# Kernel tuning notes

Hardware: AMD Instinct MI355X
Metric: run time of the kernel (lower is better)

The kernel has to match this reference:

```python
import jax, jax.numpy as jnp
import numpy as np

N = 4096
IN_SIZE = 512
MLP_W = 16
HID = 512
MID = 64  # hardcoded tgc2 output size in the torch module
OUT = 128
BN_EPS = 1e-5


def setup_inputs() -> dict:
    key = jax.random.key(0)
    ks = jax.random.split(key, 24)
    adj = (jax.random.uniform(ks[0], (N, N)) < 0.05).astype(jnp.float32)
    xdeg = jax.random.uniform(ks[1], (N, N), dtype=jnp.float32)
    ydeg = jax.random.uniform(ks[2], (N, N), dtype=jnp.float32)
    u = lambda k, sh, fan: jax.random.uniform(k, sh, jnp.float32, -1.0, 1.0) / np.sqrt(fan)
    return {
        "adj": adj, "xdeg": xdeg, "ydeg": ydeg,
        # edge MLP: 3 -> MLP_W -> 2
        "mlp_w1": u(ks[3], (3, MLP_W), 3), "mlp_b1": jnp.zeros((MLP_W,), jnp.float32),
        "mlp_w2": u(ks[4], (MLP_W, 2), MLP_W), "mlp_b2": jnp.zeros((2,), jnp.float32),
        # positional linear: Linear(N, in_size) applied to eye(N) -> pe = W^T + b
        "pe_w": u(ks[5], (N, IN_SIZE), N), "pe_b": jnp.zeros((IN_SIZE,), jnp.float32),
        # GCN weights
        "gc1_w": u(ks[6], (IN_SIZE, HID), HID),
        "lin2_w": u(ks[7], (HID, MID), HID), "lin2_b": jnp.zeros((MID,), jnp.float32),
        "gc3_w": u(ks[8], (MID, OUT), OUT),
        # BatchNorm (eval mode: running stats)
        "bn1_g": jnp.ones((HID,), jnp.float32), "bn1_b": jnp.zeros((HID,), jnp.float32),
        "bn1_m": jnp.zeros((HID,), jnp.float32), "bn1_v": jnp.ones((HID,), jnp.float32),
        "bn2_g": jnp.ones((OUT,), jnp.float32), "bn2_b": jnp.zeros((OUT,), jnp.float32),
        "bn2_m": jnp.zeros((OUT,), jnp.float32), "bn2_v": jnp.ones((OUT,), jnp.float32),
    }


def reference(adj, xdeg, ydeg, mlp_w1, mlp_b1, mlp_w2, mlp_b2, pe_w, pe_b,
              gc1_w, lin2_w, lin2_b, gc3_w,
              bn1_g, bn1_b, bn1_m, bn1_v, bn2_g, bn2_b, bn2_m, bn2_v):
    # Edge MLP + softmax over [adj, xdeg, ydeg] features; torch only computes it
    # at nonzero adj entries then scatters into a dense mask. Since the mask is
    # multiplied by adj, computing densely and multiplying is exactly equivalent.
    feats = jnp.stack([adj, xdeg, ydeg], axis=-1)          # [N, N, 3]
    h = jax.nn.relu(jnp.einsum('nmf,fw->nmw', feats, mlp_w1) + mlp_b1)
    logits = jnp.einsum('nmw,wc->nmc', h, mlp_w2) + mlp_b2  # [N, N, 2]
    mask = jax.nn.softmax(logits, axis=-1)[..., 1]          # [N, N]
    a = adj * mask + jnp.eye(adj.shape[0], dtype=adj.dtype)

    # Degree normalization: A' = D_row^{-1/2} A D_col^{-1/2} (broadcast, no diag matmuls)
    rowsum = jnp.sum(a, axis=1)
    colsum = jnp.sum(a, axis=0)
    d_row = jnp.where(rowsum > 0, rowsum ** -0.5, 0.0)
    d_col = jnp.where(colsum > 0, colsum ** -0.5, 0.0)
    a = d_row[:, None] * a * d_col[None, :]

    # pe = Linear(eye(N)) = W^T + b (eval mode, dropout off)
    pe = pe_w + pe_b[None, :]                               # [N, IN_SIZE]

    h = a @ (pe @ gc1_w)                                    # GCN layer 1
    h = (h - bn1_m) * (bn1_g / jnp.sqrt(bn1_v + BN_EPS)) + bn1_b
    h = h @ lin2_w + lin2_b                                 # tgc2
    mid = h
    h = jax.nn.relu(h)
    h = a @ (h @ gc3_w)                                     # GCN layer 3
    out = (h - bn2_m) * (bn2_g / jnp.sqrt(bn2_v + BN_EPS)) + bn2_b
    return out, mid
```

## Files before the change

### kernel.cpp

```cpp
#include <hip/hip_runtime.h>
#include <hip/hip_bf16.h>

#define NN 4096
#define INS 512
#define HIDW 512
#define MIDW 64
#define OUTW 128
#define CAP 384
#define SEG 96
#define BN_EPS 1e-5f
#define CS_BLOCKS 256
#define CS_ROWS (NN / CS_BLOCKS)
#define NSTRIP 8

__global__ __launch_bounds__(256) void k_count(
    const float* __restrict__ adj,
    unsigned long long* __restrict__ msk, int* __restrict__ cnt,
    int* __restrict__ dflag)
{
    const int t = threadIdx.x;
    const int wave = t >> 6, lane = t & 63;
    const int gw = blockIdx.x * 4 + wave;
    const int i = gw >> 3, s = gw & 7;
    const int colbase = s * 512;
    const float* __restrict__ base = adj + (size_t)i * NN + colbase + 4 * lane;
    float4 a4a = *reinterpret_cast<const float4*>(base);
    float4 a4b = *reinterpret_cast<const float4*>(base + 256);
    const float av[8] = {a4a.x, a4a.y, a4a.z, a4a.w,
                         a4b.x, a4b.y, a4b.z, a4b.w};
    unsigned long long m[8];
    int total = 0;
    #pragma unroll
    for (int c = 0; c < 8; ++c) {
        int col = colbase + ((c < 4) ? (4 * lane + c) : (256 + 4 * lane + c - 4));
        bool diag = (col == i);
        bool act = (av[c] != 0.f) || diag;
        if (diag) dflag[i] = (av[c] != 0.f) ? 1 : 0;
        m[c] = __ballot(act);
        total += __popcll(m[c]);
    }
    if (lane == 0) {
        unsigned long long* mp = msk + (size_t)gw * 8;
        #pragma unroll
        for (int c = 0; c < 8; ++c) mp[c] = m[c];
        cnt[gw] = total;
    }
}

__global__ __launch_bounds__(256) void k_fill(
    const float* __restrict__ xdeg, const float* __restrict__ ydeg,
    const unsigned long long* __restrict__ msk, const int* __restrict__ cnt,
    const int* __restrict__ dflag,
    const float* __restrict__ w1, const float* __restrict__ b1,
    const float* __restrict__ w2, const float* __restrict__ b2,
    float* __restrict__ a_vals, int* __restrict__ a_cols,
    float* __restrict__ rs_part)
{
    __shared__ float shb[16], sw1x[16], sw1y[16], sw2[32], sb2[2];
    __shared__ int   scol[4][SEG];
    __shared__ float sx[4][SEG];
    __shared__ float sy[4][SEG];
    const int t = threadIdx.x;
    const int wave = t >> 6, lane = t & 63;
    if (t < 16) {
        shb[t]  = b1[t] + w1[t];
        sw1x[t] = w1[16 + t];
        sw1y[t] = w1[32 + t];
    }
    if (t < 32) sw2[t] = w2[t];
    if (t < 2)  sb2[t] = b2[t];
    __syncthreads();

    const int gw = __builtin_amdgcn_readfirstlane(blockIdx.x * 4 + wave);
    const int i = gw >> 3, s = gw & 7;
    const int colbase = s * 512;
    const size_t rbase = (size_t)i * NN + colbase + 4 * lane;
    float4 x4a = *reinterpret_cast<const float4*>(xdeg + rbase);
    float4 x4b = *reinterpret_cast<const float4*>(xdeg + rbase + 256);
    float4 y4a = *reinterpret_cast<const float4*>(ydeg + rbase);
    float4 y4b = *reinterpret_cast<const float4*>(ydeg + rbase + 256);
    const unsigned long long* __restrict__ mp = msk + (size_t)gw * 8;
    unsigned long long mm[8];
    #pragma unroll
    for (int c = 0; c < 8; ++c) mm[c] = mp[c];
    const int* __restrict__ cb = cnt + i * NSTRIP;
    int wb = 0;
    #pragma unroll
    for (int ss = 0; ss < NSTRIP; ++ss) if (ss < s) wb += cb[ss];
    const int hasde = dflag[i];

    int bases[8];
    bases[0] = 0;
    #pragma unroll
    for (int c = 1; c < 8; ++c) bases[c] = bases[c - 1] + __popcll(mm[c - 1]);
    const int cnt_ = bases[7] + __popcll(mm[7]);
    const int n = (cnt_ < SEG) ? cnt_ : SEG;
    const unsigned long long lt = (1ULL << lane) - 1ULL;

    const float xv[8] = {x4a.x, x4a.y, x4a.z, x4a.w,
                         x4b.x, x4b.y, x4b.z, x4b.w};
    const float yv[8] = {y4a.x, y4a.y, y4a.z, y4a.w,
                         y4b.x, y4b.y, y4b.z, y4b.w};
    #pragma unroll
    for (int c = 0; c < 8; ++c) {
        if ((mm[c] >> lane) & 1ULL) {
            int pos = bases[c] + __popcll(mm[c] & lt);
            if (pos < SEG) {
                scol[wave][pos] = colbase + ((c < 4) ? (4 * lane + c)
                                                     : (256 + 4 * lane + c - 4));
                sx[wave][pos] = xv[c];
                sy[wave][pos] = yv[c];
            }
        }
    }

    float* __restrict__ gv = a_vals + (size_t)i * CAP;
    int*   __restrict__ gc = a_cols + (size_t)i * CAP;
    float local = 0.f;
    for (int p = lane; p < n; p += 64) {
        int col = scol[wave][p];
        float x = sx[wave][p], y = sy[wave][p];
        float l0 = sb2[0], l1 = sb2[1];
        #pragma unroll
        for (int w = 0; w < 16; ++w) {
            float hw = fmaf(x, sw1x[w], shb[w]);
            hw = fmaf(y, sw1y[w], hw);
            hw = fmaxf(hw, 0.f);
            l0 = fmaf(hw, sw2[2 * w],     l0);
            l1 = fmaf(hw, sw2[2 * w + 1], l1);
        }
        float v = 1.f / (1.f + __expf(l0 - l1));
        if (col == i) v = hasde ? (v + 1.f) : 1.f;
        int gp = wb + p;
        if (gp < CAP) { gc[gp] = col; gv[gp] = v; }
        local += v;
    }
    #pragma unroll
    for (int o = 32; o >= 1; o >>= 1)
        local += __shfl_down(local, o, 64);
    if (lane == 0) rs_part[gw] = local;
}

__global__ __launch_bounds__(256) void k_colsum(
    const float* __restrict__ a_vals, const int* __restrict__ a_cols,
    const int* __restrict__ cnt, float* __restrict__ P)
{
    __shared__ float ls[NN];
    const int t = threadIdx.x;
    const int b = blockIdx.x;
    for (int j = t; j < NN; j += 256) ls[j] = 0.f;
    __syncthreads();
    const int r0 = b * CS_ROWS;
    for (int r = r0; r < r0 + CS_ROWS; ++r) {
        int n = 0;
        #pragma unroll
        for (int ss = 0; ss < NSTRIP; ++ss) n += cnt[r * NSTRIP + ss];
        n = (n < CAP) ? n : CAP;
        const float* __restrict__ vr = a_vals + (size_t)r * CAP;
        const int*   __restrict__ cr = a_cols + (size_t)r * CAP;
        for (int p = t; p < n; p += 256)
            atomicAdd(&ls[cr[p]], vr[p]);
    }
    __syncthreads();
    for (int j = t; j < NN; j += 256)
        P[(size_t)b * NN + j] = ls[j];
}

__global__ __launch_bounds__(512) void k_misc(
    const float* __restrict__ lin2_w, const float* __restrict__ lin2_b,
    const float* __restrict__ bn1_g, const float* __restrict__ bn1_b,
    const float* __restrict__ bn1_m, const float* __restrict__ bn1_v,
    const float* __restrict__ bn2_g, const float* __restrict__ bn2_b,
    const float* __restrict__ bn2_m, const float* __restrict__ bn2_v,
    const float* __restrict__ rs_part, const float* __restrict__ P,
    float* __restrict__ Wp, float* __restrict__ c1,
    float* __restrict__ s2g, float* __restrict__ t2g,
    float* __restrict__ d_row, float* __restrict__ d_col)
{
    const int t = threadIdx.x;
    if (blockIdx.x == 0) {
        __shared__ float t1s[HIDW];
        {
            int h = t;
            float s1 = bn1_g[h] * rsqrtf(bn1_v[h] + BN_EPS);
            t1s[h] = bn1_b[h] - bn1_m[h] * s1;
            for (int m = 0; m < MIDW; ++m)
                Wp[(size_t)h * MIDW + m] = s1 * lin2_w[(size_t)h * MIDW + m];
        }
        __syncthreads();
        if (t < MIDW) {
            float acc = lin2_b[t];
            for (int h = 0; h < HIDW; ++h)
                acc = fmaf(t1s[h], lin2_w[(size_t)h * MIDW + t], acc);
            c1[t] = acc;
        } else if (t >= 64 && t < 64 + OUTW) {
            int j = t - 64;
            float s2 = bn2_g[j] * rsqrtf(bn2_v[j] + BN_EPS);
            s2g[j] = s2;
            t2g[j] = bn2_b[j] - bn2_m[j] * s2;
        }
    } else {
        int j = (blockIdx.x - 1) * 512 + t;
        float r = 0.f;
        #pragma unroll
        for (int s = 0; s < NSTRIP; ++s) r += rs_part[j * NSTRIP + s];
        d_row[j] = (r > 0.f) ? 1.f / sqrtf(r) : 0.f;
        float c = 0.f;
        for (int b = 0; b < CS_BLOCKS; ++b)
            c += P[(size_t)b * NN + j];
        d_col[j] = (c > 0.f) ? 1.f / sqrtf(c) : 0.f;
    }
}

template <bool ABIAS, bool ROWSCALE>
__global__ __launch_bounds__(256) void k_thin(
    const float* __restrict__ A, const float* __restrict__ B,
    const float* __restrict__ abias, const float* __restrict__ rscale,
    float* __restrict__ C, int M, int K)
{
    __shared__ float As[64][36];
    __shared__ float Bs[64][64];
    const int t = threadIdx.x;
    const int bm = blockIdx.x * 32;
    const int c2 = t & 31, rg = t >> 5;

    float acc[4][2] = {};

    for (int k0 = 0; k0 < K; k0 += 64) {
        #pragma unroll
        for (int l = 0; l < 8; ++l) {
            int e = t + l * 256;
            int r = e >> 6, k = e & 63;
            float v = A[(size_t)(bm + r) * K + k0 + k];
            if (ABIAS) v += abias[k0 + k];
            As[k][r] = v;
        }
        #pragma unroll
        for (int l = 0; l < 16; ++l) {
            int e = t + l * 256;
            int k = e >> 6, n = e & 63;
            Bs[k][n] = B[(size_t)(k0 + k) * 64 + n];
        }
        __syncthreads();
        #pragma unroll
        for (int k = 0; k < 64; ++k) {
            float4 a4 = *reinterpret_cast<const float4*>(&As[k][rg * 4]);
            float2 b2 = *reinterpret_cast<const float2*>(&Bs[k][2 * c2]);
            acc[0][0] = fmaf(a4.x, b2.x, acc[0][0]);
            acc[0][1] = fmaf(a4.x, b2.y, acc[0][1]);
            acc[1][0] = fmaf(a4.y, b2.x, acc[1][0]);
            acc[1][1] = fmaf(a4.y, b2.y, acc[1][1]);
            acc[2][0] = fmaf(a4.z, b2.x, acc[2][0]);
            acc[2][1] = fmaf(a4.z, b2.y, acc[2][1]);
            acc[3][0] = fmaf(a4.w, b2.x, acc[3][0]);
            acc[3][1] = fmaf(a4.w, b2.y, acc[3][1]);
        }
        __syncthreads();
    }

    #pragma unroll
    for (int u = 0; u < 4; ++u) {
        int r = bm + rg * 4 + u;
        float sc = ROWSCALE ? rscale[r] : 1.f;
        float2 o = make_float2(acc[u][0] * sc, acc[u][1] * sc);
        *reinterpret_cast<float2*>(&C[(size_t)r * 64 + 2 * c2]) = o;
    }
}

template <bool WITH_MID>
__global__ __launch_bounds__(256) void k_spmm(
    const float* __restrict__ a_vals, const int* __restrict__ a_cols,
    const int* __restrict__ cnt, const float* __restrict__ X,
    const float* __restrict__ d_row, const float* __restrict__ d_col,
    const float* __restrict__ c1,
    const float* __restrict__ gc3, const float* __restrict__ s2g,
    const float* __restrict__ t2g,
    float* __restrict__ O1, float* __restrict__ O2)
{
    __shared__ float sv[2][CAP];
    __shared__ int   scl[2][CAP];
    __shared__ float sacc[4][64];
    const int t = threadIdx.x;
    const int wave = t >> 6, lane = t & 63;
    const int rb = wave >> 1, h = wave & 1;
    const int i = blockIdx.x * 2 + rb;
    int n = 0;
    #pragma unroll
    for (int ss = 0; ss < NSTRIP; ++ss) n += cnt[i * NSTRIP + ss];
    n = (n < CAP) ? n : CAP;
    const int n16 = (n + 15) & ~15;
    const float* __restrict__ vrow = a_vals + (size_t)i * CAP;
    const int*   __restrict__ crow = a_cols + (size_t)i * CAP;

    for (int p = h * 64 + lane; p < n16; p += 128) {
        bool ok = p < n;
        sv[rb][p]  = ok ? vrow[p] : 0.f;
        scl[rb][p] = ok ? crow[p] : 0;
    }
    __syncthreads();

    const int eh = lane >> 5;
    const int lc = lane & 31;
    const int Q  = n16 >> 1;
    const int Qh = Q >> 1;

    float a0 = 0.f, a1 = 0.f;
    for (int q = h * Qh; q < (h + 1) * Qh; q += 4) {
        #pragma unroll
        for (int j = 0; j < 4; ++j) {
            int p = 2 * (q + j) + eh;
            float v = sv[rb][p];
            int c = scl[rb][p];
            float2 x = *reinterpret_cast<const float2*>(X + (size_t)c * 64 + 2 * lc);
            a0 = fmaf(v, x.x, a0);
            a1 = fmaf(v, x.y, a1);
        }
    }
    a0 += __shfl_xor(a0, 32);
    a1 += __shfl_xor(a1, 32);
    if (lane < 32) { sacc[wave][2 * lc] = a0; sacc[wave][2 * lc + 1] = a1; }
    __syncthreads();

    if (WITH_MID) {
        if (h == 0 && lane < 32) {
            float s0 = sacc[wave][2 * lc]     + sacc[wave + 1][2 * lc];
            float s1 = sacc[wave][2 * lc + 1] + sacc[wave + 1][2 * lc + 1];
            float dr = d_row[i];
            float dc = d_col[i];
            float m0 = fmaf(s0, dr, c1[2 * lc]);
            float m1 = fmaf(s1, dr, c1[2 * lc + 1]);
            *reinterpret_cast<float2*>(O1 + (size_t)i * 64 + 2 * lc) =
                make_float2(m0, m1);
            *reinterpret_cast<float2*>(O2 + (size_t)i * 64 + 2 * lc) =
                make_float2(dc * fmaxf(m0, 0.f), dc * fmaxf(m1, 0.f));
        }
    } else {
        if (h == 0 && lane < 32) {
            float dr = d_row[i];
            float s0 = (sacc[wave][2 * lc]     + sacc[wave + 1][2 * lc])     * dr;
            float s1 = (sacc[wave][2 * lc + 1] + sacc[wave + 1][2 * lc + 1]) * dr;
            sacc[wave][2 * lc]     = s0;
            sacc[wave][2 * lc + 1] = s1;
        }
        __syncthreads();
        const int rb2 = t >> 7;
        const int j = t & 127;
        const float* __restrict__ srow = sacc[2 * rb2];
        float acc = 0.f;
        #pragma unroll 8
        for (int k = 0; k < 64; ++k)
            acc = fmaf(srow[k], gc3[k * 128 + j], acc);
        int orow = blockIdx.x * 2 + rb2;
        O1[(size_t)orow * 128 + j] = fmaf(acc, s2g[j], t2g[j]);
    }
}

extern "C" void kernel_launch(void* const* d_in, const int* in_sizes, int n_in,
                              void* d_out, int out_size, void* d_ws, size_t ws_size,
                              hipStream_t stream) {
    const float* adj    = (const float*)d_in[0];
    const float* xdeg   = (const float*)d_in[1];
    const float* ydeg   = (const float*)d_in[2];
    const float* mlp_w1 = (const float*)d_in[3];
    const float* mlp_b1 = (const float*)d_in[4];
    const float* mlp_w2 = (const float*)d_in[5];
    const float* mlp_b2 = (const float*)d_in[6];
    const float* pe_w   = (const float*)d_in[7];
    const float* pe_b   = (const float*)d_in[8];
    const float* gc1_w  = (const float*)d_in[9];
    const float* lin2_w = (const float*)d_in[10];
    const float* lin2_b = (const float*)d_in[11];
    const float* gc3_w  = (const float*)d_in[12];
    const float* bn1_g  = (const float*)d_in[13];
    const float* bn1_b  = (const float*)d_in[14];
    const float* bn1_m  = (const float*)d_in[15];
    const float* bn1_v  = (const float*)d_in[16];
    const float* bn2_g  = (const float*)d_in[17];
    const float* bn2_b  = (const float*)d_in[18];
    const float* bn2_m  = (const float*)d_in[19];
    const float* bn2_v  = (const float*)d_in[20];

    float* out = (float*)d_out;
    float* mid = out + (size_t)NN * OUTW;

    char* w = (char*)d_ws;
    float* a_vals = (float*)w;  w += (size_t)NN * CAP * 4;
    int*   a_cols = (int*)w;    w += (size_t)NN * CAP * 4;
    unsigned long long* msk = (unsigned long long*)w; w += (size_t)NN * NSTRIP * 8 * 8;
    int*   cnt    = (int*)w;    w += (size_t)NN * NSTRIP * 4;
    int*   dflag  = (int*)w;    w += (size_t)NN * 4;
    float* rs_part= (float*)w;  w += (size_t)NN * NSTRIP * 4;
    float* d_row  = (float*)w;  w += (size_t)NN * 4;
    float* d_col  = (float*)w;  w += (size_t)NN * 4;
    float* P      = (float*)w;  w += (size_t)CS_BLOCKS * NN * 4;
    float* Wp     = (float*)w;  w += (size_t)HIDW * MIDW * 4;
    float* W2     = (float*)w;  w += (size_t)INS * MIDW * 4;
    float* c1     = (float*)w;  w += 256;
    float* s2g    = (float*)w;  w += 512;
    float* t2g    = (float*)w;  w += 512;
    float* G      = (float*)w;  w += (size_t)NN * MIDW * 4;
    float* R      = (float*)w;  w += (size_t)NN * MIDW * 4;

    k_count<<<NN * NSTRIP / 4, 256, 0, stream>>>(adj, msk, cnt, dflag);
    k_fill<<<NN * NSTRIP / 4, 256, 0, stream>>>(
        xdeg, ydeg, msk, cnt, dflag, mlp_w1, mlp_b1, mlp_w2, mlp_b2,
        a_vals, a_cols, rs_part);
    k_colsum<<<CS_BLOCKS, 256, 0, stream>>>(a_vals, a_cols, cnt, P);
    k_misc<<<9, 512, 0, stream>>>(lin2_w, lin2_b, bn1_g, bn1_b, bn1_m, bn1_v,
                                  bn2_g, bn2_b, bn2_m, bn2_v, rs_part, P,
                                  Wp, c1, s2g, t2g, d_row, d_col);
    k_thin<false, false><<<INS / 32, 256, 0, stream>>>(
        gc1_w, Wp, nullptr, nullptr, W2, INS, HIDW);
    k_thin<true, true><<<NN / 32, 256, 0, stream>>>(
        pe_w, W2, pe_b, d_col, G, NN, INS);
    k_spmm<true><<<NN / 2, 256, 0, stream>>>(
        a_vals, a_cols, cnt, G, d_row, d_col, c1,
        nullptr, nullptr, nullptr, mid, R);
    k_spmm<false><<<NN / 2, 256, 0, stream>>>(
        a_vals, a_cols, cnt, R, d_row, d_col, nullptr,
        gc3_w, s2g, t2g, out, nullptr);
}
```

Before: 135.9 us.

## Compact nonzero column indices in count pass and gather xdeg/ydeg sparsely

The count kernel now writes compacted per-strip column indices directly into a slot buffer instead of ballot bitmasks. The fill kernel uses those indices to gather xdeg and ydeg values only at active columns, rather than streaming full dense rows and compacting them through shared memory. The aim is to cut dense read traffic on the two large feature matrices. In exchange, the reads become scattered and uncoalesced, and at about 5% density most cache lines may still be touched. Strip counts are now stored capped at SEG, which changes the row write offsets slightly.

```diff
diff --git a/kernel.cpp b/kernel.cpp
--- a/kernel.cpp
+++ b/kernel.cpp
@@ -12,11 +12,11 @@
 #define CS_BLOCKS 256
 #define CS_ROWS (NN / CS_BLOCKS)
 #define NSTRIP 8
+#define SLOTCAP (NSTRIP * SEG)
 
 __global__ __launch_bounds__(256) void k_count(
     const float* __restrict__ adj,
-    unsigned long long* __restrict__ msk, int* __restrict__ cnt,
-    int* __restrict__ dflag)
+    int* __restrict__ cslot, int* __restrict__ cnt, int* __restrict__ dflag)
 {
     const int t = threadIdx.x;
     const int wave = t >> 6, lane = t & 63;
@@ -28,28 +28,28 @@
     float4 a4b = *reinterpret_cast<const float4*>(base + 256);
     const float av[8] = {a4a.x, a4a.y, a4a.z, a4a.w,
                          a4b.x, a4b.y, a4b.z, a4b.w};
-    unsigned long long m[8];
-    int total = 0;
+    int* __restrict__ slot = cslot + (size_t)i * SLOTCAP + s * SEG;
+    const unsigned long long lt = (1ULL << lane) - 1ULL;
+    int run = 0;
     #pragma unroll
     for (int c = 0; c < 8; ++c) {
         int col = colbase + ((c < 4) ? (4 * lane + c) : (256 + 4 * lane + c - 4));
         bool diag = (col == i);
         bool act = (av[c] != 0.f) || diag;
         if (diag) dflag[i] = (av[c] != 0.f) ? 1 : 0;
-        m[c] = __ballot(act);
-        total += __popcll(m[c]);
-    }
-    if (lane == 0) {
-        unsigned long long* mp = msk + (size_t)gw * 8;
-        #pragma unroll
-        for (int c = 0; c < 8; ++c) mp[c] = m[c];
-        cnt[gw] = total;
-    }
+        unsigned long long m = __ballot(act);
+        if (act) {
+            int pos = run + __popcll(m & lt);
+            if (pos < SEG) slot[pos] = col;
+        }
+        run += __popcll(m);
+    }
+    if (lane == 0) cnt[gw] = (run < SEG) ? run : SEG;
 }
 
 __global__ __launch_bounds__(256) void k_fill(
     const float* __restrict__ xdeg, const float* __restrict__ ydeg,
-    const unsigned long long* __restrict__ msk, const int* __restrict__ cnt,
+    const int* __restrict__ cslot, const int* __restrict__ cnt,
     const int* __restrict__ dflag,
     const float* __restrict__ w1, const float* __restrict__ b1,
     const float* __restrict__ w2, const float* __restrict__ b2,
@@ -57,9 +57,6 @@
     float* __restrict__ rs_part)
 {
     __shared__ float shb[16], sw1x[16], sw1y[16], sw2[32], sb2[2];
-    __shared__ int   scol[4][SEG];
-    __shared__ float sx[4][SEG];
-    __shared__ float sy[4][SEG];
     const int t = threadIdx.x;
     const int wave = t >> 6, lane = t & 63;
     if (t < 16) {
@@ -73,53 +70,23 @@
 
     const int gw = __builtin_amdgcn_readfirstlane(blockIdx.x * 4 + wave);
     const int i = gw >> 3, s = gw & 7;
-    const int colbase = s * 512;
-    const size_t rbase = (size_t)i * NN + colbase + 4 * lane;
-    float4 x4a = *reinterpret_cast<const float4*>(xdeg + rbase);
-    float4 x4b = *reinterpret_cast<const float4*>(xdeg + rbase + 256);
-    float4 y4a = *reinterpret_cast<const float4*>(ydeg + rbase);
-    float4 y4b = *reinterpret_cast<const float4*>(ydeg + rbase + 256);
-    const unsigned long long* __restrict__ mp = msk + (size_t)gw * 8;
-    unsigned long long mm[8];
-    #pragma unroll
-    for (int c = 0; c < 8; ++c) mm[c] = mp[c];
     const int* __restrict__ cb = cnt + i * NSTRIP;
     int wb = 0;
     #pragma unroll
     for (int ss = 0; ss < NSTRIP; ++ss) if (ss < s) wb += cb[ss];
+    const int n = cb[s];
     const int hasde = dflag[i];
-
-    int bases[8];
-    bases[0] = 0;
-    #pragma unroll
-    for (int c = 1; c < 8; ++c) bases[c] = bases[c - 1] + __popcll(mm[c - 1]);
-    const int cnt_ = bases[7] + __popcll(mm[7]);
-    const int n = (cnt_ < SEG) ? cnt_ : SEG;
-    const unsigned long long lt = (1ULL << lane) - 1ULL;
-
-    const float xv[8] = {x4a.x, x4a.y, x4a.z, x4a.w,
-                         x4b.x, x4b.y, x4b.z, x4b.w};
-    const float yv[8] = {y4a.x, y4a.y, y4a.z, y4a.w,
-                         y4b.x, y4b.y, y4b.z, y4b.w};
-    #pragma unroll
-    for (int c = 0; c < 8; ++c) {
-        if ((mm[c] >> lane) & 1ULL) {
-            int pos = bases[c] + __popcll(mm[c] & lt);
-            if (pos < SEG) {
-                scol[wave][pos] = colbase + ((c < 4) ? (4 * lane + c)
-                                                     : (256 + 4 * lane + c - 4));
-                sx[wave][pos] = xv[c];
-                sy[wave][pos] = yv[c];
-            }
-        }
-    }
-
+    const int* __restrict__ slot = cslot + (size_t)i * SLOTCAP + s * SEG;
+    const float* __restrict__ xrow = xdeg + (size_t)i * NN;
+    const float* __restrict__ yrow = ydeg + (size_t)i * NN;
     float* __restrict__ gv = a_vals + (size_t)i * CAP;
     int*   __restrict__ gc = a_cols + (size_t)i * CAP;
+
     float local = 0.f;
     for (int p = lane; p < n; p += 64) {
-        int col = scol[wave][p];
-        float x = sx[wave][p], y = sy[wave][p];
+        int col = slot[p];
+        float x = xrow[col];
+        float y = yrow[col];
         float l0 = sb2[0], l1 = sb2[1];
         #pragma unroll
         for (int w = 0; w < 16; ++w) {
@@ -386,7 +353,7 @@
     char* w = (char*)d_ws;
     float* a_vals = (float*)w;  w += (size_t)NN * CAP * 4;
     int*   a_cols = (int*)w;    w += (size_t)NN * CAP * 4;
-    unsigned long long* msk = (unsigned long long*)w; w += (size_t)NN * NSTRIP * 8 * 8;
+    int*   cslot  = (int*)w;    w += (size_t)NN * SLOTCAP * 4;
     int*   cnt    = (int*)w;    w += (size_t)NN * NSTRIP * 4;
     int*   dflag  = (int*)w;    w += (size_t)NN * 4;
     float* rs_part= (float*)w;  w += (size_t)NN * NSTRIP * 4;
@@ -401,9 +368,9 @@
     float* G      = (float*)w;  w += (size_t)NN * MIDW * 4;
     float* R      = (float*)w;  w += (size_t)NN * MIDW * 4;
 
-    k_count<<<NN * NSTRIP / 4, 256, 0, stream>>>(adj, msk, cnt, dflag);
+    k_count<<<NN * NSTRIP / 4, 256, 0, stream>>>(adj, cslot, cnt, dflag);
     k_fill<<<NN * NSTRIP / 4, 256, 0, stream>>>(
-        xdeg, ydeg, msk, cnt, dflag, mlp_w1, mlp_b1, mlp_w2, mlp_b2,
+        xdeg, ydeg, cslot, cnt, dflag, mlp_w1, mlp_b1, mlp_w2, mlp_b2,
         a_vals, a_cols, rs_part);
     k_colsum<<<CS_BLOCKS, 256, 0, stream>>>(a_vals, a_cols, cnt, P);
     k_misc<<<9, 512, 0, stream>>>(lin2_w, lin2_b, bn1_g, bn1_b, bn1_m, bn1_v,
```

Result: no change. 137.4 us (+1.2%).
